# Kernel tuning notes

Measured on AMD Instinct MI355X. Metric: run time of the kernel, lower is better.

Reference implementation:

```python
import jax, jax.numpy as jnp
import numpy as np
from jax import lax

NUM_LAYERS = 1000
DIM = 10
BATCH = 2_000_000


def setup_inputs() -> dict:
    key = jax.random.key(0)
    kx, kw, kb = jax.random.split(key, 3)
    x = jax.random.normal(kx, (BATCH, DIM), dtype=jnp.float32)
    # torch Linear weight is [out, in]; stack all 1000 layers: [L, out, in]
    # std = 1/sqrt(DIM) keeps activation scale roughly stable across 1000 layers
    Ws = jax.random.normal(kw, (NUM_LAYERS, DIM, DIM), dtype=jnp.float32) * (DIM ** -0.5)
    bs = jax.random.normal(kb, (NUM_LAYERS, DIM), dtype=jnp.float32) * 0.01
    return {"x": x, "Ws": Ws, "bs": bs}


def reference(x, Ws, bs):
    # Sequential of 1000 Linear(10,10): h <- h @ W_l.T + b_l, no activation.
    def step(h, wb):
        W, b = wb  # W: [out, in], b: [out]
        return h @ W.T + b, None
    out, _ = lax.scan(step, x, (Ws, bs))
    return out
```

## Files before the change

kernel.cpp:

```cpp
#include <hip/hip_runtime.h>

#define NUM_LAYERS 1000
#define DIM 10
#define STRIDE 112
#define LPB 16
#define NBLK 63
#define TILE_Q4 1280

__device__ inline void compose_one(const float* __restrict__ src,
                                   float* __restrict__ dst,
                                   int c, int lane) {
    const float* F = src + (size_t)(2 * c) * STRIDE;
    const float* G = src + (size_t)(2 * c + 1) * STRIDE;
    float colf[DIM], o[DIM];
    #pragma unroll
    for (int r = 0; r < DIM; ++r) colf[r] = F[lane * DIM + r];
    #pragma unroll
    for (int r = 0; r < DIM; ++r) {
        float acc = (lane == DIM) ? G[100 + r] : 0.f;
        #pragma unroll
        for (int k = 0; k < DIM; ++k)
            acc += G[k * DIM + r] * colf[k];
        o[r] = acc;
    }
    float* D = dst + (size_t)c * STRIDE;
    #pragma unroll
    for (int r = 0; r < DIM; ++r) D[lane * DIM + r] = o[r];
}

__global__ __launch_bounds__(1024) void compose_fused(const float* __restrict__ Ws,
                                                      const float* __restrict__ bs,
                                                      float* __restrict__ wsout,
                                                      float* __restrict__ aff,
                                                      unsigned int* __restrict__ counter) {
    __shared__ float A[64 * STRIDE];
    __shared__ float B[32 * STRIDE];
    __shared__ unsigned int s_last;
    const int tid = threadIdx.x;
    const int blk = blockIdx.x;

    for (int e = tid; e < LPB * 100; e += 1024) {
        int ll = e / 100, rem = e % 100;
        int r = rem / 10, k = rem % 10;
        int l = blk * LPB + ll;
        float v = (l < NUM_LAYERS) ? Ws[(size_t)l * 100 + rem]
                                   : (r == k ? 1.f : 0.f);
        A[ll * STRIDE + k * DIM + r] = v;
    }
    for (int e = tid; e < LPB * DIM; e += 1024) {
        int ll = e / DIM, r = e % DIM;
        int l = blk * LPB + ll;
        float v = (l < NUM_LAYERS) ? bs[(size_t)l * DIM + r] : 0.f;
        A[ll * STRIDE + 100 + r] = v;
    }

    const int wave = tid >> 6, lane = tid & 63;
    {
        const float* src = A;
        float* dst = B;
        for (int n = LPB / 2; n >= 1; n >>= 1) {
            __syncthreads();
            if (wave < n && lane <= DIM) compose_one(src, dst, wave, lane);
            const float* t = dst; dst = (float*)src; src = t;
        }
    }
    __syncthreads();
    if (tid < 110) wsout[(size_t)blk * STRIDE + tid] = A[tid];

    __threadfence();
    __syncthreads();
    if (tid == 0) s_last = atomicAdd(counter, 1u);
    __syncthreads();
    if (s_last != NBLK - 1) return;

    __threadfence();
    for (int e = tid; e < 64 * STRIDE; e += 1024) {
        int chunk = e / STRIDE, pos = e % STRIDE;
        float v;
        if (pos >= 110)        v = 0.f;
        else if (chunk < NBLK) v = __hip_atomic_load(&wsout[(size_t)chunk * STRIDE + pos],
                                                     __ATOMIC_RELAXED,
                                                     __HIP_MEMORY_SCOPE_AGENT);
        else v = (pos < 100 && (pos / 10 == pos % 10)) ? 1.f : 0.f;
        A[e] = v;
    }
    {
        const float* src = A;
        float* dst = B;
        for (int n = 32; n >= 1; n >>= 1) {
            __syncthreads();
            if (lane <= DIM)
                for (int c = wave; c < n; c += 16)
                    compose_one(src, dst, c, lane);
            const float* t = dst; dst = (float*)src; src = t;
        }
    }
    __syncthreads();
    if (tid < 110) {
        if (tid < 100) {
            int j = tid / DIM, r = tid % DIM;
            aff[r * DIM + j] = A[tid];
        } else {
            aff[tid] = A[tid];
        }
    }
}

__global__ __launch_bounds__(256) void apply_affine(const float* __restrict__ x,
                                                    const float* __restrict__ aff,
                                                    float* __restrict__ out,
                                                    int nq4) {
    __shared__ float4 lds4[TILE_Q4];
    __shared__ float s[112];
    const int tid = threadIdx.x;
    if (tid < 112) s[tid] = (tid < 110) ? aff[tid] : 0.f;

    const int q0 = blockIdx.x * TILE_Q4;
    const float4* __restrict__ xin = (const float4*)x;
    float4* __restrict__ op = (float4*)out;

    #pragma unroll
    for (int i = 0; i < 5; ++i) {
        int q = q0 + i * 256 + tid;
        if (q < nq4) lds4[i * 256 + tid] = xin[q];
    }
    __syncthreads();

    if (q0 + 5 * tid + 5 <= nq4) {
        float xv[20];
        #pragma unroll
        for (int i = 0; i < 5; ++i) {
            float4 v = lds4[5 * tid + i];
            xv[4 * i + 0] = v.x; xv[4 * i + 1] = v.y;
            xv[4 * i + 2] = v.z; xv[4 * i + 3] = v.w;
        }
        float o[20];
        #pragma unroll
        for (int rr = 0; rr < 2; ++rr) {
            #pragma unroll
            for (int j = 0; j < DIM; ++j) {
                float acc = s[100 + j];
                #pragma unroll
                for (int k = 0; k < DIM; ++k)
                    acc += s[j * DIM + k] * xv[rr * DIM + k];
                o[rr * DIM + j] = acc;
            }
        }
        #pragma unroll
        for (int i = 0; i < 5; ++i)
            lds4[5 * tid + i] = make_float4(o[4 * i + 0], o[4 * i + 1],
                                            o[4 * i + 2], o[4 * i + 3]);
    }
    __syncthreads();

    #pragma unroll
    for (int i = 0; i < 5; ++i) {
        int q = q0 + i * 256 + tid;
        if (q < nq4) op[q] = lds4[i * 256 + tid];
    }
}

extern "C" void kernel_launch(void* const* d_in, const int* in_sizes, int n_in,
                              void* d_out, int out_size, void* d_ws, size_t ws_size,
                              hipStream_t stream) {
    const float* x  = (const float*)d_in[0];
    const float* Ws = (const float*)d_in[1];
    const float* bs = (const float*)d_in[2];
    float* out = (float*)d_out;

    float* ws_chunks = (float*)d_ws;
    float* ws_aff    = ws_chunks + NBLK * STRIDE;
    unsigned int* ws_counter = (unsigned int*)(ws_aff + STRIDE);

    hipMemsetAsync(ws_counter, 0, sizeof(unsigned int), stream);

    compose_fused<<<NBLK, 1024, 0, stream>>>(Ws, bs, ws_chunks, ws_aff, ws_counter);

    const int nq4 = in_sizes[0] / 4;
    const int blocks = (nq4 + TILE_Q4 - 1) / TILE_Q4;
    apply_affine<<<blocks, 256, 0, stream>>>(x, ws_aff, out, nq4);
}
```

Before: 188.1 us.

## Single-block layer composition and persistent prefetching apply kernel with nontemporal stores

```diff
diff --git a/kernel.cpp b/kernel.cpp
--- a/kernel.cpp
+++ b/kernel.cpp
@@ -2,161 +2,221 @@
 
 #define NUM_LAYERS 1000
 #define DIM 10
-#define STRIDE 112
-#define LPB 16
-#define NBLK 63
+#define CL 8
+#define NCH 125
+#define SLOT 111
 #define TILE_Q4 1280
-
-__device__ inline void compose_one(const float* __restrict__ src,
-                                   float* __restrict__ dst,
-                                   int c, int lane) {
-    const float* F = src + (size_t)(2 * c) * STRIDE;
-    const float* G = src + (size_t)(2 * c + 1) * STRIDE;
-    float colf[DIM], o[DIM];
-    #pragma unroll
-    for (int r = 0; r < DIM; ++r) colf[r] = F[lane * DIM + r];
-    #pragma unroll
-    for (int r = 0; r < DIM; ++r) {
-        float acc = (lane == DIM) ? G[100 + r] : 0.f;
+#define APPLY_BLOCKS 1536
+
+typedef float f32x4 __attribute__((ext_vector_type(4)));
+
+__global__ __launch_bounds__(256, 1) void compose_all(const float* __restrict__ Ws,
+                                                      const float* __restrict__ bs,
+                                                      float* __restrict__ aff) {
+    __shared__ float A[NCH * SLOT];
+    __shared__ float B[((NCH + 1) / 2) * SLOT];
+    const int tid = threadIdx.x;
+
+    if (tid < NCH) {
+        const int t = tid;
+        const float4* __restrict__ W4 = (const float4*)Ws + (size_t)t * CL * 25;
+
+        float Rc[DIM][DIM];
+        float bv[DIM];
+
+        {
+            float m[100];
+            #pragma unroll
+            for (int i = 0; i < 25; ++i) {
+                float4 v = W4[i];
+                m[4*i+0] = v.x; m[4*i+1] = v.y; m[4*i+2] = v.z; m[4*i+3] = v.w;
+            }
+            #pragma unroll
+            for (int j = 0; j < DIM; ++j)
+                #pragma unroll
+                for (int r = 0; r < DIM; ++r)
+                    Rc[j][r] = m[r * 10 + j];
+            #pragma unroll
+            for (int r = 0; r < DIM; ++r)
+                bv[r] = bs[(size_t)t * CL * 10 + r];
+        }
+
         #pragma unroll
-        for (int k = 0; k < DIM; ++k)
-            acc += G[k * DIM + r] * colf[k];
-        o[r] = acc;
-    }
-    float* D = dst + (size_t)c * STRIDE;
-    #pragma unroll
-    for (int r = 0; r < DIM; ++r) D[lane * DIM + r] = o[r];
-}
-
-__global__ __launch_bounds__(1024) void compose_fused(const float* __restrict__ Ws,
-                                                      const float* __restrict__ bs,
-                                                      float* __restrict__ wsout,
-                                                      float* __restrict__ aff,
-                                                      unsigned int* __restrict__ counter) {
-    __shared__ float A[64 * STRIDE];
-    __shared__ float B[32 * STRIDE];
-    __shared__ unsigned int s_last;
-    const int tid = threadIdx.x;
-    const int blk = blockIdx.x;
-
-    for (int e = tid; e < LPB * 100; e += 1024) {
-        int ll = e / 100, rem = e % 100;
-        int r = rem / 10, k = rem % 10;
-        int l = blk * LPB + ll;
-        float v = (l < NUM_LAYERS) ? Ws[(size_t)l * 100 + rem]
-                                   : (r == k ? 1.f : 0.f);
-        A[ll * STRIDE + k * DIM + r] = v;
-    }
-    for (int e = tid; e < LPB * DIM; e += 1024) {
-        int ll = e / DIM, r = e % DIM;
-        int l = blk * LPB + ll;
-        float v = (l < NUM_LAYERS) ? bs[(size_t)l * DIM + r] : 0.f;
-        A[ll * STRIDE + 100 + r] = v;
-    }
-
-    const int wave = tid >> 6, lane = tid & 63;
-    {
-        const float* src = A;
-        float* dst = B;
-        for (int n = LPB / 2; n >= 1; n >>= 1) {
-            __syncthreads();
-            if (wave < n && lane <= DIM) compose_one(src, dst, wave, lane);
-            const float* t = dst; dst = (float*)src; src = t;
-        }
-    }
-    __syncthreads();
-    if (tid < 110) wsout[(size_t)blk * STRIDE + tid] = A[tid];
-
-    __threadfence();
-    __syncthreads();
-    if (tid == 0) s_last = atomicAdd(counter, 1u);
-    __syncthreads();
-    if (s_last != NBLK - 1) return;
-
-    __threadfence();
-    for (int e = tid; e < 64 * STRIDE; e += 1024) {
-        int chunk = e / STRIDE, pos = e % STRIDE;
-        float v;
-        if (pos >= 110)        v = 0.f;
-        else if (chunk < NBLK) v = __hip_atomic_load(&wsout[(size_t)chunk * STRIDE + pos],
-                                                     __ATOMIC_RELAXED,
-                                                     __HIP_MEMORY_SCOPE_AGENT);
-        else v = (pos < 100 && (pos / 10 == pos % 10)) ? 1.f : 0.f;
-        A[e] = v;
-    }
-    {
-        const float* src = A;
-        float* dst = B;
-        for (int n = 32; n >= 1; n >>= 1) {
-            __syncthreads();
-            if (lane <= DIM)
-                for (int c = wave; c < n; c += 16)
-                    compose_one(src, dst, c, lane);
-            const float* t = dst; dst = (float*)src; src = t;
-        }
+        for (int s = 1; s < CL; ++s) {
+            float m[100];
+            #pragma unroll
+            for (int i = 0; i < 25; ++i) {
+                float4 v = W4[s * 25 + i];
+                m[4*i+0] = v.x; m[4*i+1] = v.y; m[4*i+2] = v.z; m[4*i+3] = v.w;
+            }
+            #pragma unroll
+            for (int j = 0; j < DIM; ++j) {
+                float tmp[DIM];
+                #pragma unroll
+                for (int r = 0; r < DIM; ++r) {
+                    float acc = 0.f;
+                    #pragma unroll
+                    for (int k = 0; k < DIM; ++k)
+                        acc += m[r * 10 + k] * Rc[j][k];
+                    tmp[r] = acc;
+                }
+                #pragma unroll
+                for (int r = 0; r < DIM; ++r) Rc[j][r] = tmp[r];
+            }
+            float tb[DIM];
+            #pragma unroll
+            for (int r = 0; r < DIM; ++r) {
+                float acc = bs[((size_t)t * CL + s) * 10 + r];
+                #pragma unroll
+                for (int k = 0; k < DIM; ++k)
+                    acc += m[r * 10 + k] * bv[k];
+                tb[r] = acc;
+            }
+            #pragma unroll
+            for (int r = 0; r < DIM; ++r) bv[r] = tb[r];
+        }
+
+        #pragma unroll
+        for (int j = 0; j < DIM; ++j)
+            #pragma unroll
+            for (int r = 0; r < DIM; ++r)
+                A[t * SLOT + j * 10 + r] = Rc[j][r];
+        #pragma unroll
+        for (int r = 0; r < DIM; ++r)
+            A[t * SLOT + 100 + r] = bv[r];
+    }
+
+    const float* src = A;
+    float* dst = B;
+    int n = NCH;
+    while (n > 1) {
+        int half = (n + 1) >> 1;
+        __syncthreads();
+        if (tid < 253) {
+            const int j = tid % 11;
+            for (int d = tid / 11; d < half; d += 23) {
+                const float* F = src + (size_t)(2 * d) * SLOT;
+                float o[DIM];
+                if (2 * d + 1 < n) {
+                    const float* G = F + SLOT;
+                    float colf[DIM];
+                    #pragma unroll
+                    for (int r = 0; r < DIM; ++r) colf[r] = F[j * 10 + r];
+                    #pragma unroll
+                    for (int r = 0; r < DIM; ++r) {
+                        float acc = (j == DIM) ? G[100 + r] : 0.f;
+                        #pragma unroll
+                        for (int k = 0; k < DIM; ++k)
+                            acc += G[k * 10 + r] * colf[k];
+                        o[r] = acc;
+                    }
+                } else {
+                    #pragma unroll
+                    for (int r = 0; r < DIM; ++r) o[r] = F[j * 10 + r];
+                }
+                float* D = dst + (size_t)d * SLOT;
+                #pragma unroll
+                for (int r = 0; r < DIM; ++r) D[j * 10 + r] = o[r];
+            }
+        }
+        n = half;
+        float* t2 = dst; dst = (float*)src; src = t2;
     }
     __syncthreads();
     if (tid < 110) {
         if (tid < 100) {
             int j = tid / DIM, r = tid % DIM;
-            aff[r * DIM + j] = A[tid];
+            aff[r * DIM + j] = src[tid];
         } else {
-            aff[tid] = A[tid];
+            aff[tid] = src[tid];
         }
     }
 }
 
-__global__ __launch_bounds__(256) void apply_affine(const float* __restrict__ x,
-                                                    const float* __restrict__ aff,
-                                                    float* __restrict__ out,
-                                                    int nq4) {
+__global__ __launch_bounds__(256, 6) void apply_affine(const float* __restrict__ x,
+                                                       const float* __restrict__ aff,
+                                                       float* __restrict__ out,
+                                                       int nq4, int ntiles) {
     __shared__ float4 lds4[TILE_Q4];
     __shared__ float s[112];
     const int tid = threadIdx.x;
+    int tile = blockIdx.x;
+    if (tile >= ntiles) return;
+
     if (tid < 112) s[tid] = (tid < 110) ? aff[tid] : 0.f;
 
-    const int q0 = blockIdx.x * TILE_Q4;
     const float4* __restrict__ xin = (const float4*)x;
-    float4* __restrict__ op = (float4*)out;
-
-    #pragma unroll
-    for (int i = 0; i < 5; ++i) {
-        int q = q0 + i * 256 + tid;
-        if (q < nq4) lds4[i * 256 + tid] = xin[q];
+    f32x4* __restrict__ op = (f32x4*)out;
+
+    float4 r0, r1, r2, r3, r4;
+    int q0 = tile * TILE_Q4;
+    {
+        int q;
+        q = q0 + 0 * 256 + tid; if (q < nq4) r0 = xin[q];
+        q = q0 + 1 * 256 + tid; if (q < nq4) r1 = xin[q];
+        q = q0 + 2 * 256 + tid; if (q < nq4) r2 = xin[q];
+        q = q0 + 3 * 256 + tid; if (q < nq4) r3 = xin[q];
+        q = q0 + 4 * 256 + tid; if (q < nq4) r4 = xin[q];
     }
     __syncthreads();
 
-    if (q0 + 5 * tid + 5 <= nq4) {
-        float xv[20];
-        #pragma unroll
-        for (int i = 0; i < 5; ++i) {
-            float4 v = lds4[5 * tid + i];
-            xv[4 * i + 0] = v.x; xv[4 * i + 1] = v.y;
-            xv[4 * i + 2] = v.z; xv[4 * i + 3] = v.w;
-        }
-        float o[20];
-        #pragma unroll
-        for (int rr = 0; rr < 2; ++rr) {
-            #pragma unroll
-            for (int j = 0; j < DIM; ++j) {
-                float acc = s[100 + j];
-                #pragma unroll
-                for (int k = 0; k < DIM; ++k)
-                    acc += s[j * DIM + k] * xv[rr * DIM + k];
-                o[rr * DIM + j] = acc;
-            }
-        }
-        #pragma unroll
-        for (int i = 0; i < 5; ++i)
-            lds4[5 * tid + i] = make_float4(o[4 * i + 0], o[4 * i + 1],
-                                            o[4 * i + 2], o[4 * i + 3]);
-    }
-    __syncthreads();
-
-    #pragma unroll
-    for (int i = 0; i < 5; ++i) {
-        int q = q0 + i * 256 + tid;
-        if (q < nq4) op[q] = lds4[i * 256 + tid];
+    for (;;) {
+        lds4[0 * 256 + tid] = r0;
+        lds4[1 * 256 + tid] = r1;
+        lds4[2 * 256 + tid] = r2;
+        lds4[3 * 256 + tid] = r3;
+        lds4[4 * 256 + tid] = r4;
+        __syncthreads();
+
+        const int q0c = tile * TILE_Q4;
+        const int nt = tile + gridDim.x;
+        if (nt < ntiles) {
+            q0 = nt * TILE_Q4;
+            int q;
+            q = q0 + 0 * 256 + tid; if (q < nq4) r0 = xin[q];
+            q = q0 + 1 * 256 + tid; if (q < nq4) r1 = xin[q];
+            q = q0 + 2 * 256 + tid; if (q < nq4) r2 = xin[q];
+            q = q0 + 3 * 256 + tid; if (q < nq4) r3 = xin[q];
+            q = q0 + 4 * 256 + tid; if (q < nq4) r4 = xin[q];
+        }
+
+        if (q0c + 5 * tid + 5 <= nq4) {
+            float xv[20];
+            #pragma unroll
+            for (int i = 0; i < 5; ++i) {
+                float4 v = lds4[5 * tid + i];
+                xv[4*i+0] = v.x; xv[4*i+1] = v.y; xv[4*i+2] = v.z; xv[4*i+3] = v.w;
+            }
+            float o[20];
+            #pragma unroll
+            for (int rr = 0; rr < 2; ++rr)
+                #pragma unroll
+                for (int j = 0; j < DIM; ++j) {
+                    float acc = s[100 + j];
+                    #pragma unroll
+                    for (int k = 0; k < DIM; ++k)
+                        acc += s[j * DIM + k] * xv[rr * DIM + k];
+                    o[rr * DIM + j] = acc;
+                }
+            #pragma unroll
+            for (int i = 0; i < 5; ++i)
+                lds4[5 * tid + i] = make_float4(o[4*i+0], o[4*i+1], o[4*i+2], o[4*i+3]);
+        }
+        __syncthreads();
+
+        {
+            const f32x4* l4 = (const f32x4*)lds4;
+            int q;
+            q = q0c + 0 * 256 + tid; if (q < nq4) __builtin_nontemporal_store(l4[0 * 256 + tid], &op[q]);
+            q = q0c + 1 * 256 + tid; if (q < nq4) __builtin_nontemporal_store(l4[1 * 256 + tid], &op[q]);
+            q = q0c + 2 * 256 + tid; if (q < nq4) __builtin_nontemporal_store(l4[2 * 256 + tid], &op[q]);
+            q = q0c + 3 * 256 + tid; if (q < nq4) __builtin_nontemporal_store(l4[3 * 256 + tid], &op[q]);
+            q = q0c + 4 * 256 + tid; if (q < nq4) __builtin_nontemporal_store(l4[4 * 256 + tid], &op[q]);
+        }
+
+        tile = nt;
+        if (tile >= ntiles) break;
+        __syncthreads();
     }
 }
 
@@ -168,15 +228,12 @@
     const float* bs = (const float*)d_in[2];
     float* out = (float*)d_out;
 
-    float* ws_chunks = (float*)d_ws;
-    float* ws_aff    = ws_chunks + NBLK * STRIDE;
-    unsigned int* ws_counter = (unsigned int*)(ws_aff + STRIDE);
-
-    hipMemsetAsync(ws_counter, 0, sizeof(unsigned int), stream);
-
-    compose_fused<<<NBLK, 1024, 0, stream>>>(Ws, bs, ws_chunks, ws_aff, ws_counter);
+    float* ws_aff = (float*)d_ws;
+
+    compose_all<<<1, 256, 0, stream>>>(Ws, bs, ws_aff);
 
     const int nq4 = in_sizes[0] / 4;
-    const int blocks = (nq4 + TILE_Q4 - 1) / TILE_Q4;
-    apply_affine<<<blocks, 256, 0, stream>>>(x, ws_aff, out, nq4);
+    const int ntiles = (nq4 + TILE_Q4 - 1) / TILE_Q4;
+    const int nblk = (ntiles < APPLY_BLOCKS) ? ntiles : APPLY_BLOCKS;
+    apply_affine<<<nblk, 256, 0, stream>>>(x, ws_aff, out, nq4, ntiles);
 }
```

New measurement: 213.7 us. 1.14x slower.
